# Kernel tuning notes

Measured on AMD Instinct MI355X. Metric: run time of the kernel, lower is better.

Reference implementation:

```python
import jax, jax.numpy as jnp
import numpy as np

H, HK, D, BLK, GH = 32, 8, 96, 64, 128   # q heads, kv heads, head_dim, gate block, gate hidden
HIDDEN = 3072
THR = 0.03
NEG = -1e30

def _rot_half(x):
    h = x.shape[-1] // 2
    return jnp.concatenate([-x[..., h:], x[..., :h]], axis=-1)

def setup_inputs() -> dict:
    key = jax.random.key(0)
    ks = jax.random.split(key, 6)
    B, S = 1, 2048
    hidden_states = jax.random.normal(ks[0], (B, S, HIDDEN), dtype=jnp.float32)
    # RoPE tables, theta = 10000
    inv_freq = 1.0 / (10000.0 ** (np.arange(0, D, 2, dtype=np.float32) / D))
    t = np.arange(S, dtype=np.float32)
    freqs = np.outer(t, inv_freq)                   # [S, D/2]
    emb = np.concatenate([freqs, freqs], axis=-1)   # [S, D]
    cos = jnp.asarray(np.cos(emb), dtype=jnp.float32)
    sin = jnp.asarray(np.sin(emb), dtype=jnp.float32)
    op = H * D + 2 * HK * D
    qkv_w = jax.random.normal(ks[1], (HIDDEN, op), dtype=jnp.float32) * 0.02
    o_w = jax.random.normal(ks[2], (H * D, HIDDEN), dtype=jnp.float32) * 0.02
    gate_wq = jax.random.normal(ks[3], (D, GH), dtype=jnp.float32) * 0.05
    gate_wk = jax.random.normal(ks[4], (2 * D, GH), dtype=jnp.float32) * 0.05
    return dict(hidden_states=hidden_states, cos=cos, sin=sin,
                qkv_w=qkv_w, o_w=o_w, gate_wq=gate_wq, gate_wk=gate_wk)

def reference(hidden_states, cos, sin, qkv_w, o_w, gate_wq, gate_wk):
    B, S, _ = hidden_states.shape
    G = H // HK            # GQA group size
    nB = S // BLK          # number of gate blocks
    scale = D ** -0.5

    # fused QKV projection and head split
    qkv = hidden_states @ qkv_w
    q = qkv[..., : H * D].reshape(B, S, H, D)
    k = qkv[..., H * D : H * D + HK * D].reshape(B, S, HK, D)
    v = qkv[..., H * D + HK * D :].reshape(B, S, HK, D)
    q_nope, k_nope = q, k

    # RoPE (unsqueeze over head dim)
    cs = cos[None, :, None, :]
    sn = sin[None, :, None, :]
    q = q * cs + _rot_half(q) * sn
    k = k * cs + _rot_half(k) * sn

    # ---- learned block-sparse gate (SeerAttention AttnGate) ----
    kb = k_nope.reshape(B, nB, BLK, HK, D)
    k_pool = jnp.concatenate([kb.mean(2), kb.max(2)], axis=-1)      # [B,nB,HK,2D] avg+max seq pooling
    k_gate = jnp.einsum('bnhe,eg->bnhg', k_pool, gate_wk)
    q_pool = q_nope.reshape(B, S, HK, G, D).mean(3)                 # q-head pooling to kv heads
    q_pool = q_pool.reshape(B, nB, BLK, HK, D).mean(2)              # block pooling
    q_gate = jnp.einsum('bnhd,dg->bnhg', q_pool, gate_wq)
    gate_logits = jnp.einsum('bqhg,bkhg->bhqk', q_gate, k_gate) * (GH ** -0.5)
    blk_causal = jnp.tril(jnp.ones((nB, nB), dtype=bool))
    gate_logits = jnp.where(blk_causal, gate_logits, NEG)
    gate_probs = jax.nn.softmax(gate_logits, axis=-1)
    block_mask = (gate_probs >= THR) & blk_causal                   # threshold sparsity method
    block_mask = block_mask | jnp.eye(nB, dtype=bool)               # diagonal block always active

    # expand block mask to token level, intersect with causal mask
    tok_mask = jnp.repeat(jnp.repeat(block_mask, BLK, axis=2), BLK, axis=3)  # [B,HK,S,S]
    causal = jnp.tril(jnp.ones((S, S), dtype=bool))
    mask = tok_mask & causal

    # ---- block-sparse masked attention with GQA ----
    qh = q.transpose(0, 2, 1, 3).reshape(B, HK, G, S, D)
    kh = k.transpose(0, 2, 1, 3)                                    # [B,HK,S,D]
    vh = v.transpose(0, 2, 1, 3)
    scores = jnp.einsum('bhgsd,bhtd->bhgst', qh, kh) * scale
    scores = jnp.where(mask[:, :, None], scores, NEG)
    attn = jax.nn.softmax(scores, axis=-1)
    out = jnp.einsum('bhgst,bhtd->bhgsd', attn, vh)                 # [B,HK,G,S,D]
    out = out.reshape(B, H, S, D).transpose(0, 2, 1, 3).reshape(B, S, H * D)
    return out @ o_w
```

## Files before the change

### kernel.cpp

```cpp
#include <hip/hip_runtime.h>
#include <hip/hip_bf16.h>
#include <math.h>

#define S_LEN 2048
#define HID 3072
#define NHEAD 32
#define NKV 8
#define HDIM 96
#define QKV_N 4608
#define NB 32
#define GHDIM 128
#define KOFF 3072
#define VOFF 3840

typedef __attribute__((ext_vector_type(8))) short bf16x8;
typedef __attribute__((ext_vector_type(4))) short bf16x4;
typedef __attribute__((ext_vector_type(4))) float f32x4;
typedef unsigned short ushort_t;

#define SCALE2 0.14724444754f

__device__ __forceinline__ unsigned short f2bf(float x) {
    unsigned u = __float_as_uint(x);
    u += 0x7fffu + ((u >> 16) & 1u);
    return (unsigned short)(u >> 16);
}
__device__ __forceinline__ unsigned packbf2(float a, float b) {
    return (unsigned)f2bf(a) | ((unsigned)f2bf(b) << 16);
}
__device__ __forceinline__ float bf2f(ushort_t u) {
    return __uint_as_float(((unsigned)u) << 16);
}

#define GLOBAL_AS __attribute__((address_space(1)))
#define LDS_AS __attribute__((address_space(3)))
__device__ __forceinline__ void gl_lds16(const void* g, void* l) {
    __builtin_amdgcn_global_load_lds((const GLOBAL_AS unsigned int*)g,
                                     (LDS_AS unsigned int*)l, 16, 0, 0);
}
__device__ __forceinline__ void barrier_raw() {
    asm volatile("s_barrier" ::: "memory");
}

__global__ __launch_bounds__(256, 4) void gemm_bf16(const ushort_t* __restrict__ A,
                                                    const ushort_t* __restrict__ Bt,
                                                    float* __restrict__ C,
                                                    ushort_t* __restrict__ Cbf,
                                                    float* __restrict__ CfK,
                                                    int M, int N, int K, int mode) {
    __shared__ ushort_t As[2][128 * 64];
    __shared__ ushort_t Bs[2][128 * 64];
    const int tid = threadIdx.x;
    const int lane = tid & 63;
    const int w = tid >> 6;
    const int wm = (w >> 1) * 64;
    const int wn = (w & 1) * 64;
    const int l15 = lane & 15;
    const int quad = lane >> 4;

    const int nbx = (int)gridDim.x;
    const int nwg = nbx * (int)gridDim.y;
    const int bid = (int)blockIdx.y * nbx + (int)blockIdx.x;
    const int cpx = nwg >> 3;
    const int swz = (bid & 7) * cpx + (bid >> 3);
    const int m0 = (swz / nbx) * 128;
    const int n0 = (swz % nbx) * 128;

    f32x4 acc[4][4] = {};

    auto stage = [&](int k0, int buf) {
#pragma unroll
        for (int j = 0; j < 4; ++j) {
            int s = j * 256 + w * 64 + lane;
            int row = s >> 3;
            int kc = (s & 7) ^ (row & 7);
            gl_lds16(A + (size_t)(m0 + row) * K + k0 + kc * 8,
                     &As[buf][(j * 256 + w * 64) * 8]);
        }
#pragma unroll
        for (int j = 0; j < 4; ++j) {
            int s = j * 256 + w * 64 + lane;
            int row = s >> 3;
            int kc = (s & 7) ^ (row & 7);
            gl_lds16(Bt + (size_t)(n0 + row) * K + k0 + kc * 8,
                     &Bs[buf][(j * 256 + w * 64) * 8]);
        }
    };

    stage(0, 0);
    int cur = 0;

    for (int k0 = 0; k0 < K; k0 += 64) {
        if (k0 + 64 < K) {
            stage(k0 + 64, cur ^ 1);
            asm volatile("s_waitcnt vmcnt(8)" ::: "memory");
        } else {
            asm volatile("s_waitcnt vmcnt(0)" ::: "memory");
        }
        barrier_raw();

        const ushort_t* Asc = As[cur];
        const ushort_t* Bsc = Bs[cur];
        bf16x8 af[2][4], bf[2][4];
#pragma unroll
        for (int mt = 0; mt < 4; ++mt) {
            int row = wm + mt * 16 + l15;
            int rx = row & 7;
#pragma unroll
            for (int ph = 0; ph < 2; ++ph)
                af[ph][mt] = *(const bf16x8*)&Asc[(row * 8 + ((ph * 4 + quad) ^ rx)) * 8];
        }
#pragma unroll
        for (int nt = 0; nt < 4; ++nt) {
            int row = wn + nt * 16 + l15;
            int rx = row & 7;
#pragma unroll
            for (int ph = 0; ph < 2; ++ph)
                bf[ph][nt] = *(const bf16x8*)&Bsc[(row * 8 + ((ph * 4 + quad) ^ rx)) * 8];
        }
#pragma unroll
        for (int ph = 0; ph < 2; ++ph)
#pragma unroll
            for (int mt = 0; mt < 4; ++mt)
#pragma unroll
                for (int nt = 0; nt < 4; ++nt)
                    acc[mt][nt] = __builtin_amdgcn_mfma_f32_16x16x32_bf16(
                        af[ph][mt], bf[ph][nt], acc[mt][nt], 0, 0, 0);

        barrier_raw();
        cur ^= 1;
    }

    if (mode == 0) {
#pragma unroll
        for (int mt = 0; mt < 4; ++mt)
#pragma unroll
            for (int nt = 0; nt < 4; ++nt)
#pragma unroll
                for (int r = 0; r < 4; ++r) {
                    int row = m0 + wm + mt * 16 + quad * 4 + r;
                    int col = n0 + wn + nt * 16 + l15;
                    C[(size_t)row * N + col] = acc[mt][nt][r];
                }
    } else {
        const bool isK = (n0 >= KOFF) && (n0 < VOFF);
#pragma unroll
        for (int mt = 0; mt < 4; ++mt)
#pragma unroll
            for (int nt = 0; nt < 4; ++nt)
#pragma unroll
                for (int r = 0; r < 4; ++r) {
                    int row = m0 + wm + mt * 16 + quad * 4 + r;
                    int col = n0 + wn + nt * 16 + l15;
                    Cbf[(size_t)row * N + col] = f2bf(acc[mt][nt][r]);
                    if (isK) CfK[(size_t)row * 768 + col - KOFF] = acc[mt][nt][r];
                }
    }
}

__device__ __forceinline__ void conv_body(const float* __restrict__ X,
                                          ushort_t* __restrict__ Y, int i) {
    const float4 v = *(const float4*)(X + (size_t)i * 4);
    int2 p;
    p.x = (int)packbf2(v.x, v.y);
    p.y = (int)packbf2(v.z, v.w);
    *(int2*)(Y + (size_t)i * 4) = p;
}

__device__ __forceinline__ void transpose_body(const float* __restrict__ W,
                                               ushort_t* __restrict__ Wt,
                                               int K, int N, int k0, int n0, int tid) {
    __shared__ float Ts[64][65];
    {
        int r = tid >> 2, cq = tid & 3;
#pragma unroll
        for (int i = 0; i < 4; ++i) {
            int c = cq * 16 + i * 4;
            const float4 v = *(const float4*)(W + (size_t)(k0 + r) * N + n0 + c);
            Ts[r][c] = v.x; Ts[r][c + 1] = v.y; Ts[r][c + 2] = v.z; Ts[r][c + 3] = v.w;
        }
    }
    __syncthreads();
#pragma unroll
    for (int it = 0; it < 2; ++it) {
        int n = (tid >> 3) + it * 32;
        int kc = tid & 7;
        int4 r;
        r.x = (int)(packbf2(Ts[kc * 8 + 0][n], Ts[kc * 8 + 1][n]));
        r.y = (int)(packbf2(Ts[kc * 8 + 2][n], Ts[kc * 8 + 3][n]));
        r.z = (int)(packbf2(Ts[kc * 8 + 4][n], Ts[kc * 8 + 5][n]));
        r.w = (int)(packbf2(Ts[kc * 8 + 6][n], Ts[kc * 8 + 7][n]));
        *(int4*)(Wt + (size_t)(n0 + n) * K + k0 + kc * 8) = r;
    }
}

__global__ __launch_bounds__(256) void prep1(const float* __restrict__ hidden,
                                             ushort_t* __restrict__ h_bf,
                                             const float* __restrict__ qkv_w,
                                             ushort_t* __restrict__ w1t) {
    int id = blockIdx.x;
    int tid = threadIdx.x;
    if (id < 6144) {
        conv_body(hidden, h_bf, id * 256 + tid);
    } else {
        int r = id - 6144;
        transpose_body(qkv_w, w1t, HID, QKV_N, (r / 72) * 64, (r % 72) * 64, tid);
    }
}

__global__ __launch_bounds__(256) void prep2(const ushort_t* __restrict__ qkv_bf,
                                             const float* __restrict__ cosb,
                                             const float* __restrict__ sinb,
                                             ushort_t* __restrict__ Qb,
                                             ushort_t* __restrict__ Kb,
                                             ushort_t* __restrict__ Vtb,
                                             const float* __restrict__ o_w,
                                             ushort_t* __restrict__ o_wt) {
    int id = blockIdx.x;
    int tid = threadIdx.x;
    if (id < 15360) {
        int idx = id * 256 + tid;
        int d = idx % 48;
        int tmp = idx / 48;
        int head = tmp % 40;
        int s = tmp / 40;
        float c0 = cosb[s * 96 + d], c1 = cosb[s * 96 + d + 48];
        float s0 = sinb[s * 96 + d], s1 = sinb[s * 96 + d + 48];
        if (head < 32) {
            size_t base = (size_t)s * QKV_N + head * 96;
            float x0 = bf2f(qkv_bf[base + d]), x1 = bf2f(qkv_bf[base + d + 48]);
            size_t ob = (size_t)s * HID + head * 96;
            Qb[ob + d] = f2bf((x0 * c0 - x1 * s0) * SCALE2);
            Qb[ob + d + 48] = f2bf((x1 * c1 + x0 * s1) * SCALE2);
        } else {
            int hh = head - 32;
            size_t base = (size_t)s * QKV_N + KOFF + hh * 96;
            float x0 = bf2f(qkv_bf[base + d]), x1 = bf2f(qkv_bf[base + d + 48]);
            size_t ob = ((size_t)hh * S_LEN + s) * 96;
            Kb[ob + d] = f2bf(x0 * c0 - x1 * s0);
            Kb[ob + d + 48] = f2bf(x1 * c1 + x0 * s1);
        }
    } else if (id < 15616) {
        int r = id - 15360;
        int ibk = r & 31, h = r >> 5;
        __shared__ ushort_t Vs[64][104];
        {
            int rr = tid >> 2, seg = tid & 3;
#pragma unroll
            for (int j = 0; j < 3; ++j) {
                int c = seg * 24 + j * 8;
                const int4 v = *(const int4*)(qkv_bf + (size_t)(ibk * 64 + rr) * QKV_N +
                                              VOFF + h * 96 + c);
                *(int4*)&Vs[rr][c] = v;
            }
        }
        __syncthreads();
#pragma unroll
        for (int it = 0; it < 3; ++it) {
            int s = tid + it * 256;
            int d = s >> 3, tc = s & 7;
            int4 o;
            o.x = (int)Vs[tc * 8 + 0][d] | ((int)Vs[tc * 8 + 1][d] << 16);
            o.y = (int)Vs[tc * 8 + 2][d] | ((int)Vs[tc * 8 + 3][d] << 16);
            o.z = (int)Vs[tc * 8 + 4][d] | ((int)Vs[tc * 8 + 5][d] << 16);
            o.w = (int)Vs[tc * 8 + 6][d] | ((int)Vs[tc * 8 + 7][d] << 16);
            *(int4*)(Vtb + ((size_t)h * 96 + d) * S_LEN + ibk * 64 + tc * 8) = o;
        }
    } else {
        int r = id - 15616;
        transpose_body(o_w, o_wt, HID, HID, (r / 48) * 64, (r % 48) * 64, tid);
    }
}

__global__ __launch_bounds__(256) void pool_gate_kernel(const float* __restrict__ qkvK,
                                                        const ushort_t* __restrict__ qkv_bf,
                                                        const float* __restrict__ gate_wk,
                                                        const float* __restrict__ gate_wq,
                                                        float* __restrict__ k_gate,
                                                        float* __restrict__ q_gate) {
    int nb = blockIdx.x, h = blockIdx.y;
    int tid = threadIdx.x;
    __shared__ float poolk[192];
    __shared__ float poolq[96];
    if (tid < 128) {
        if (tid < 96) {
            float s = 0.f, mx = -1e30f;
            for (int i = 0; i < 64; i++) {
                float v = qkvK[(size_t)(nb * 64 + i) * 768 + h * 96 + tid];
                s += v;
                mx = fmaxf(mx, v);
            }
            poolk[tid] = s * (1.f / 64.f);
            poolk[96 + tid] = mx;
        }
    } else {
        int t2 = tid - 128;
        if (t2 < 96) {
            float s = 0.f;
            for (int i = 0; i < 64; i++)
#pragma unroll
                for (int g = 0; g < 4; g++)
                    s += bf2f(qkv_bf[(size_t)(nb * 64 + i) * QKV_N + (h * 4 + g) * 96 + t2]);
            poolq[t2] = s * (1.f / 256.f);
        }
    }
    __syncthreads();
    if (tid < 128) {
        float acc = 0.f;
        for (int e = 0; e < 192; e++) acc += poolk[e] * gate_wk[e * GHDIM + tid];
        k_gate[(size_t)(nb * NKV + h) * GHDIM + tid] = acc;
    } else {
        int t2 = tid - 128;
        float acc = 0.f;
        for (int e = 0; e < 96; e++) acc += poolq[e] * gate_wq[e * GHDIM + t2];
        q_gate[(size_t)(nb * NKV + h) * GHDIM + t2] = acc;
    }
}

__global__ __launch_bounds__(64) void blockmask_kernel(const float* __restrict__ q_gate,
                                                       const float* __restrict__ k_gate,
                                                       int* __restrict__ mask) {
    int h = blockIdx.x, qb = blockIdx.y;
    int tid = threadIdx.x;
    __shared__ float logits[32];
    if (tid < 32) {
        if (tid <= qb) {
            float acc = 0.f;
            const float* qg = &q_gate[(size_t)(qb * NKV + h) * GHDIM];
            const float* kg = &k_gate[(size_t)(tid * NKV + h) * GHDIM];
            for (int e = 0; e < GHDIM; e++) acc += qg[e] * kg[e];
            logits[tid] = acc * 0.08838834764831845f;
        } else {
            logits[tid] = -1e30f;
        }
    }
    __syncthreads();
    if (tid < 32) {
        float mx = -1e30f;
        for (int j = 0; j <= qb; j++) mx = fmaxf(mx, logits[j]);
        float sum = 0.f;
        for (int j = 0; j <= qb; j++) sum += __expf(logits[j] - mx);
        float p = (tid <= qb) ? __expf(logits[tid] - mx) / sum : 0.f;
        int m = ((p >= 0.03f) && (tid <= qb)) || (tid == qb);
        mask[(h * NB + qb) * NB + tid] = m;
    }
}

__global__ __launch_bounds__(256) void attn_mfma(const ushort_t* __restrict__ Qb,
                                                 const ushort_t* __restrict__ Kb,
                                                 const ushort_t* __restrict__ Vtb,
                                                 const int* __restrict__ mask,
                                                 ushort_t* __restrict__ out) {
    const int hq = blockIdx.x;
    const int ib = NB - 1 - (int)blockIdx.y;
    const int h = hq >> 2;
    const int tid = threadIdx.x;
    const int lane = tid & 63;
    const int w = tid >> 6;
    const int l15 = lane & 15;
    const int quad = lane >> 4;

    __shared__ ushort_t KsL[2][64 * 96];
    __shared__ ushort_t VtL[2][96 * 64];

    int pk[3];
    {
        int b0 = quad + (l15 & 7);
#pragma unroll
        for (int ks = 0; ks < 3; ++ks) {
            int p = b0 + ks * 4;
            if (p >= 12) p -= 12;
            if (p >= 12) p -= 12;
            pk[ks] = p;
        }
    }

    bf16x8 qf[3];
    {
        const ushort_t* qp = Qb + (size_t)(ib * 64 + w * 16 + l15) * HID + hq * 96;
#pragma unroll
        for (int ks = 0; ks < 3; ++ks)
            qf[ks] = *(const bf16x8*)(qp + ks * 32 + quad * 8);
    }

    const ushort_t* kbase = Kb + (size_t)h * S_LEN * 96;
    const ushort_t* vbase = Vtb + (size_t)h * 96 * S_LEN;

    unsigned long long bits =
        __ballot((lane <= ib) && (mask[(h * NB + ib) * NB + (lane & 31)] != 0));

    float m_i = -1e30f, l_i = 0.f;
    f32x4 acc_o[6] = {};

    auto stage = [&](int jb, int buf) {
#pragma unroll
        for (int j = 0; j < 3; ++j) {
            int s = j * 256 + w * 64 + lane;
            int t = (s * 2731) >> 15;
            int cpos = s - t * 12;
            int c = cpos - (t & 7);
            if (c < 0) c += 12;
            gl_lds16(kbase + (size_t)(jb * 64 + t) * 96 + c * 8,
                     &KsL[buf][(j * 256 + w * 64) * 8]);
        }
#pragma unroll
        for (int j = 0; j < 3; ++j) {
            int s = j * 256 + w * 64 + lane;
            int d = s >> 3;
            int tc = (s & 7) ^ (d & 7);
            gl_lds16(vbase + (size_t)d * S_LEN + jb * 64 + tc * 8,
                     &VtL[buf][(j * 256 + w * 64) * 8]);
        }
    };

    int jb = (int)__builtin_ctzll(bits);
    bits &= bits - 1;
    stage(jb, 0);
    int cur = 0;

    while (true) {
        int jn = -1;
        if (bits) {
            jn = (int)__builtin_ctzll(bits);
            bits &= bits - 1;
        }
        if (jn >= 0) {
            stage(jn, cur ^ 1);
            asm volatile("s_waitcnt vmcnt(6)" ::: "memory");
        } else {
            asm volatile("s_waitcnt vmcnt(0)" ::: "memory");
        }
        barrier_raw();

        const ushort_t* Kc = KsL[cur];
        const ushort_t* Vc = VtL[cur];

        f32x4 st[4] = {};
#pragma unroll
        for (int ks = 0; ks < 3; ++ks)
#pragma unroll
            for (int nt = 0; nt < 4; ++nt) {
                bf16x8 kb = *(const bf16x8*)&Kc[(nt * 16 + l15) * 96 + pk[ks] * 8];
                st[nt] = __builtin_amdgcn_mfma_f32_16x16x32_bf16(kb, qf[ks], st[nt], 0, 0, 0);
            }
        if (jb == ib) {
            int q = w * 16 + l15;
#pragma unroll
            for (int nt = 0; nt < 4; ++nt)
#pragma unroll
                for (int r = 0; r < 4; ++r)
                    if ((nt * 16 + quad * 4 + r) > q) st[nt][r] = -1e30f;
        }
        float mx = -1e30f;
#pragma unroll
        for (int nt = 0; nt < 4; ++nt)
#pragma unroll
            for (int r = 0; r < 4; ++r) mx = fmaxf(mx, st[nt][r]);
        mx = fmaxf(mx, __shfl_xor(mx, 16));
        mx = fmaxf(mx, __shfl_xor(mx, 32));
        float mnew = fmaxf(m_i, mx);
        float alpha = __builtin_amdgcn_exp2f(m_i - mnew);
        float ps = 0.f;
#pragma unroll
        for (int nt = 0; nt < 4; ++nt)
#pragma unroll
            for (int r = 0; r < 4; ++r) {
                float p = __builtin_amdgcn_exp2f(st[nt][r] - mnew);
                st[nt][r] = p;
                ps += p;
            }
        ps += __shfl_xor(ps, 16);
        ps += __shfl_xor(ps, 32);
        l_i = l_i * alpha + ps;
        m_i = mnew;
#pragma unroll
        for (int t = 0; t < 6; ++t)
#pragma unroll
            for (int r = 0; r < 4; ++r) acc_o[t][r] *= alpha;
        bf16x4 pf[4];
#pragma unroll
        for (int kblk = 0; kblk < 4; ++kblk) {
            union { bf16x4 v; unsigned u[2]; } pb;
            pb.u[0] = packbf2(st[kblk][0], st[kblk][1]);
            pb.u[1] = packbf2(st[kblk][2], st[kblk][3]);
            pf[kblk] = pb.v;
        }
#pragma unroll
        for (int kblk = 0; kblk < 4; ++kblk) {
            int cchunk = kblk * 2 + (quad >> 1);
            int eoff = (quad & 1) * 4;
#pragma unroll
            for (int dt = 0; dt < 6; ++dt) {
                int d = dt * 16 + l15;
                bf16x4 vf = *(const bf16x4*)&Vc[(d * 8 + (cchunk ^ (d & 7))) * 8 + eoff];
                acc_o[dt] = __builtin_amdgcn_mfma_f32_16x16x16bf16_1k(
                    vf, pf[kblk], acc_o[dt], 0, 0, 0);
            }
        }

        if (jn < 0) break;
        asm volatile("s_waitcnt lgkmcnt(0)" ::: "memory");
        barrier_raw();
        jb = jn;
        cur ^= 1;
    }

    float inv = 1.f / l_i;
    size_t orow = (size_t)(ib * 64 + w * 16 + l15) * HID + hq * 96;
#pragma unroll
    for (int dt = 0; dt < 6; ++dt) {
        int2 pkd;
        pkd.x = (int)packbf2(acc_o[dt][0] * inv, acc_o[dt][1] * inv);
        pkd.y = (int)packbf2(acc_o[dt][2] * inv, acc_o[dt][3] * inv);
        *(int2*)(out + orow + dt * 16 + quad * 4) = pkd;
    }
}

extern "C" void kernel_launch(void* const* d_in, const int* in_sizes, int n_in,
                              void* d_out, int out_size, void* d_ws, size_t ws_size,
                              hipStream_t stream) {
    const float* hidden  = (const float*)d_in[0];
    const float* cosb    = (const float*)d_in[1];
    const float* sinb    = (const float*)d_in[2];
    const float* qkv_w   = (const float*)d_in[3];
    const float* o_w     = (const float*)d_in[4];
    const float* gate_wq = (const float*)d_in[5];
    const float* gate_wk = (const float*)d_in[6];
    float* out = (float*)d_out;

    char* ws = (char*)d_ws;
    ushort_t* qkv_bf   = (ushort_t*)ws;
    float*    qkv_f32K = (float*)(ws + 18874368);
    ushort_t* h_bf     = (ushort_t*)(ws + 25165824);
    ushort_t* w1t      = (ushort_t*)(ws + 37748736);
    ushort_t* attn_out = (ushort_t*)(ws + 66060288);
    ushort_t* Kb       = (ushort_t*)(ws + 78643200);
    ushort_t* Vtb      = (ushort_t*)(ws + 81788928);
    float*    k_gate   = (float*)(ws + 84934656);
    float*    q_gate   = (float*)(ws + 85065728);
    int*      mask     = (int*)(ws + 85196800);
    ushort_t* Qb   = h_bf;
    ushort_t* o_wt = w1t;

    prep1<<<9600, 256, 0, stream>>>(hidden, h_bf, qkv_w, w1t);
    gemm_bf16<<<dim3(QKV_N / 128, S_LEN / 128), 256, 0, stream>>>(
        h_bf, w1t, nullptr, qkv_bf, qkv_f32K, S_LEN, QKV_N, HID, 1);
    pool_gate_kernel<<<dim3(NB, NKV), 256, 0, stream>>>(qkv_f32K, qkv_bf,
                                                        gate_wk, gate_wq, k_gate, q_gate);
    blockmask_kernel<<<dim3(NKV, NB), 64, 0, stream>>>(q_gate, k_gate, mask);
    prep2<<<17920, 256, 0, stream>>>(qkv_bf, cosb, sinb, Qb, Kb, Vtb, o_w, o_wt);
    attn_mfma<<<dim3(NHEAD, NB), 256, 0, stream>>>(Qb, Kb, Vtb, mask, attn_out);
    gemm_bf16<<<dim3(HID / 128, S_LEN / 128), 256, 0, stream>>>(
        attn_out, o_wt, out, nullptr, nullptr, S_LEN, HID, HID, 0);
}
```

Measured before the change: 416.7 us.

## Halve GEMM K-tile to 32 with two-row swizzled LDS layout and drop block swizzle

Cuts the GEMM K step from 64 to 32, halving LDS per buffer and packing two 32-wide rows into each 64-element swizzled LDS line so reads stay bank-conflict free. It also removes the XCD-aware workgroup remapping and uses plain blockIdx tiling. The aim is likely lower LDS use for higher occupancy, at the cost of twice as many barriers and loop iterations and possibly worse L2 locality across XCDs.

```diff
diff --git a/kernel.cpp b/kernel.cpp
--- a/kernel.cpp
+++ b/kernel.cpp
@@ -48,8 +48,8 @@
                                                     ushort_t* __restrict__ Cbf,
                                                     float* __restrict__ CfK,
                                                     int M, int N, int K, int mode) {
-    __shared__ ushort_t As[2][128 * 64];
-    __shared__ ushort_t Bs[2][128 * 64];
+    __shared__ ushort_t As[2][128 * 32];
+    __shared__ ushort_t Bs[2][128 * 32];
     const int tid = threadIdx.x;
     const int lane = tid & 63;
     const int w = tid >> 6;
@@ -57,31 +57,29 @@
     const int wn = (w & 1) * 64;
     const int l15 = lane & 15;
     const int quad = lane >> 4;
-
-    const int nbx = (int)gridDim.x;
-    const int nwg = nbx * (int)gridDim.y;
-    const int bid = (int)blockIdx.y * nbx + (int)blockIdx.x;
-    const int cpx = nwg >> 3;
-    const int swz = (bid & 7) * cpx + (bid >> 3);
-    const int m0 = (swz / nbx) * 128;
-    const int n0 = (swz % nbx) * 128;
+    const int m0 = blockIdx.y * 128;
+    const int n0 = blockIdx.x * 128;
 
     f32x4 acc[4][4] = {};
 
     auto stage = [&](int k0, int buf) {
 #pragma unroll
-        for (int j = 0; j < 4; ++j) {
+        for (int j = 0; j < 2; ++j) {
             int s = j * 256 + w * 64 + lane;
-            int row = s >> 3;
-            int kc = (s & 7) ^ (row & 7);
+            int line = s >> 3;
+            int seg8 = (s & 7) ^ (line & 7);
+            int row = 2 * line + (seg8 >> 2);
+            int kc = seg8 & 3;
             gl_lds16(A + (size_t)(m0 + row) * K + k0 + kc * 8,
                      &As[buf][(j * 256 + w * 64) * 8]);
         }
 #pragma unroll
-        for (int j = 0; j < 4; ++j) {
+        for (int j = 0; j < 2; ++j) {
             int s = j * 256 + w * 64 + lane;
-            int row = s >> 3;
-            int kc = (s & 7) ^ (row & 7);
+            int line = s >> 3;
+            int seg8 = (s & 7) ^ (line & 7);
+            int row = 2 * line + (seg8 >> 2);
+            int kc = seg8 & 3;
             gl_lds16(Bt + (size_t)(n0 + row) * K + k0 + kc * 8,
                      &Bs[buf][(j * 256 + w * 64) * 8]);
         }
@@ -90,10 +88,10 @@
     stage(0, 0);
     int cur = 0;
 
-    for (int k0 = 0; k0 < K; k0 += 64) {
-        if (k0 + 64 < K) {
-            stage(k0 + 64, cur ^ 1);
-            asm volatile("s_waitcnt vmcnt(8)" ::: "memory");
+    for (int k0 = 0; k0 < K; k0 += 32) {
+        if (k0 + 32 < K) {
+            stage(k0 + 32, cur ^ 1);
+            asm volatile("s_waitcnt vmcnt(4)" ::: "memory");
         } else {
             asm volatile("s_waitcnt vmcnt(0)" ::: "memory");
         }
@@ -101,31 +99,27 @@
 
         const ushort_t* Asc = As[cur];
         const ushort_t* Bsc = Bs[cur];
-        bf16x8 af[2][4], bf[2][4];
+        bf16x8 af[4], bfr[4];
 #pragma unroll
         for (int mt = 0; mt < 4; ++mt) {
-            int row = wm + mt * 16 + l15;
-            int rx = row & 7;
-#pragma unroll
-            for (int ph = 0; ph < 2; ++ph)
-                af[ph][mt] = *(const bf16x8*)&Asc[(row * 8 + ((ph * 4 + quad) ^ rx)) * 8];
+            int r = wm + mt * 16 + l15;
+            int line = r >> 1;
+            int pos = ((((r & 1) << 2) | quad) ^ (line & 7));
+            af[mt] = *(const bf16x8*)&Asc[(line * 8 + pos) * 8];
         }
 #pragma unroll
         for (int nt = 0; nt < 4; ++nt) {
-            int row = wn + nt * 16 + l15;
-            int rx = row & 7;
-#pragma unroll
-            for (int ph = 0; ph < 2; ++ph)
-                bf[ph][nt] = *(const bf16x8*)&Bsc[(row * 8 + ((ph * 4 + quad) ^ rx)) * 8];
-        }
-#pragma unroll
-        for (int ph = 0; ph < 2; ++ph)
-#pragma unroll
-            for (int mt = 0; mt < 4; ++mt)
-#pragma unroll
-                for (int nt = 0; nt < 4; ++nt)
-                    acc[mt][nt] = __builtin_amdgcn_mfma_f32_16x16x32_bf16(
-                        af[ph][mt], bf[ph][nt], acc[mt][nt], 0, 0, 0);
+            int r = wn + nt * 16 + l15;
+            int line = r >> 1;
+            int pos = ((((r & 1) << 2) | quad) ^ (line & 7));
+            bfr[nt] = *(const bf16x8*)&Bsc[(line * 8 + pos) * 8];
+        }
+#pragma unroll
+        for (int mt = 0; mt < 4; ++mt)
+#pragma unroll
+            for (int nt = 0; nt < 4; ++nt)
+                acc[mt][nt] = __builtin_amdgcn_mfma_f32_16x16x32_bf16(
+                    af[mt], bfr[nt], acc[mt][nt], 0, 0, 0);
 
         barrier_raw();
         cur ^= 1;
```

Result: faster. 399.9 us (-4.0%).
